# Optimization experiments

Hardware: AMD Instinct MI355X
Metric: run time of the kernel (lower is better)

## Reference

```python
import jax, jax.numpy as jnp
import numpy as np

B, T, C = 256, 168, 1024
N_SEQ = 168
HORIZON = 24


def setup_inputs() -> dict:
    key = jax.random.key(0)
    k1, k2, k3, k4 = jax.random.split(key, 4)
    x = jax.random.normal(k1, (B, T, C), dtype=jnp.float32)
    y = jax.random.normal(k2, (B, T, C), dtype=jnp.float32)
    # nn.Linear(n_seq, 1): weight [1, n_seq], bias [1]
    w = jax.random.normal(k3, (1, N_SEQ), dtype=jnp.float32) / jnp.sqrt(jnp.float32(N_SEQ))
    b = jax.random.normal(k4, (1,), dtype=jnp.float32) * 0.01
    return {"x": x, "y": y, "w": w, "b": b}


def reference(x, y, w, b):
    # x is unused in the original torch forward.
    n_seq = w.shape[1]
    yt = jnp.transpose(y, (0, 2, 1))          # [B, C, T]
    buf0 = yt[:, :, -n_seq:]                  # rolling window [B, C, n_seq]
    wv = w[0]                                 # [n_seq]
    bv = b[0]

    def step(buf, _):
        pred = jnp.einsum('bcn,n->bc', buf, wv) + bv   # [B, C]
        buf = jnp.concatenate([buf[:, :, 1:], pred[:, :, None]], axis=2)
        return buf, pred

    _, preds = jax.lax.scan(step, buf0, None, length=HORIZON)  # [H, B, C]
    # equivalent to y[:, :, -horizon:].permute(0, 2, 1) -> [B, H, C]
    return jnp.transpose(preds, (1, 0, 2))
```

## Files before the change

### kernel.cpp

```cpp
#include <hip/hip_runtime.h>

#define B_ 256
#define T_ 168
#define C_ 1024
#define H_ 24


__global__ __launch_bounds__(192) void ar_precompute(const float* __restrict__ w,
                                                     const float* __restrict__ bias,
                                                     float* __restrict__ ws) {
    __shared__ float lw[T_];
    const int t = threadIdx.x;
    if (t < T_) lw[t] = w[t];
    __syncthreads();
    if (t < T_) {
        float col[H_];
        #pragma unroll
        for (int k = 0; k < H_; ++k) {
            float v = (t >= k) ? lw[t - k] : 0.0f;
            #pragma unroll
            for (int j = 0; j < k; ++j)
                v += lw[T_ - k + j] * col[j];
            col[k] = v;
        }
        #pragma unroll
        for (int k = 0; k < H_; ++k)
            ws[t * H_ + k] = col[k];
    } else if (t == T_) {
        float bv = bias[0];
        float beta[H_];
        #pragma unroll
        for (int k = 0; k < H_; ++k) {
            float v = bv;
            #pragma unroll
            for (int j = 0; j < k; ++j)
                v += lw[T_ - k + j] * beta[j];
            beta[k] = v;
        }
        #pragma unroll
        for (int k = 0; k < H_; ++k)
            ws[T_ * H_ + k] = beta[k];
    }
}

__global__ __launch_bounds__(256) void ar_main(const float* __restrict__ y,
                                               const float* __restrict__ ws,
                                               float* __restrict__ out) {
    const int c = blockIdx.x * 256 + threadIdx.x;
    const int b = blockIdx.y;
    const float* __restrict__ yp = y + (size_t)b * (size_t)(T_ * C_) + c;
    const float* __restrict__ beta = ws + T_ * H_;

    float acc[H_];
    #pragma unroll
    for (int k = 0; k < H_; ++k) acc[k] = beta[k];

    #pragma unroll 4
    for (int t = 0; t < T_; ++t) {
        const float yv = yp[(size_t)t * C_];
        const float4* __restrict__ w4 = (const float4*)(ws + t * H_);
        #pragma unroll
        for (int q = 0; q < H_ / 4; ++q) {
            const float4 wv = w4[q];
            acc[4 * q + 0] += wv.x * yv;
            acc[4 * q + 1] += wv.y * yv;
            acc[4 * q + 2] += wv.z * yv;
            acc[4 * q + 3] += wv.w * yv;
        }
    }

    float* __restrict__ op = out + ((size_t)b * H_) * C_ + c;
    #pragma unroll
    for (int k = 0; k < H_; ++k)
        op[(size_t)k * C_] = acc[k];
}

extern "C" void kernel_launch(void* const* d_in, const int* in_sizes, int n_in,
                              void* d_out, int out_size, void* d_ws, size_t ws_size,
                              hipStream_t stream) {
    const float* y    = (const float*)d_in[1];
    const float* w    = (const float*)d_in[2];
    const float* bias = (const float*)d_in[3];
    float* out = (float*)d_out;
    float* ws  = (float*)d_ws;

    ar_precompute<<<1, 192, 0, stream>>>(w, bias, ws);
    ar_main<<<dim3(C_ / 256, B_), 256, 0, stream>>>(y, ws, out);
}
```

Measured before the change: 44.22 us.

## Fuse weight-propagation precompute into main kernel with shared-memory coefficients

Merges the single-block precompute kernel into the main kernel, so every block recomputes the unrolled horizon coefficient matrix and bias terms into shared memory before accumulating. This removes one kernel launch, the serial dependency between launches and the global workspace round trip. In exchange, each of the 1024 blocks redundantly does the O(T·H²) precompute, which adds per-block latency before the streaming loop, and the coefficient reads now come from LDS instead of cached global memory.

```diff
diff --git a/kernel.cpp b/kernel.cpp
--- a/kernel.cpp
+++ b/kernel.cpp
@@ -5,19 +5,23 @@
 #define C_ 1024
 #define H_ 24
 
+__global__ __launch_bounds__(256) void ar_fused(const float* __restrict__ y,
+                                                const float* __restrict__ w,
+                                                const float* __restrict__ bias,
+                                                float* __restrict__ out) {
+    __shared__ float lw[T_];
+    __shared__ float sW[T_ * H_];
+    __shared__ float sbeta[H_];
 
-__global__ __launch_bounds__(192) void ar_precompute(const float* __restrict__ w,
-                                                     const float* __restrict__ bias,
-                                                     float* __restrict__ ws) {
-    __shared__ float lw[T_];
-    const int t = threadIdx.x;
-    if (t < T_) lw[t] = w[t];
+    const int tid = threadIdx.x;
+    if (tid < T_) lw[tid] = w[tid];
     __syncthreads();
-    if (t < T_) {
+
+    if (tid < T_) {
         float col[H_];
         #pragma unroll
         for (int k = 0; k < H_; ++k) {
-            float v = (t >= k) ? lw[t - k] : 0.0f;
+            float v = (tid >= k) ? lw[tid - k] : 0.0f;
             #pragma unroll
             for (int j = 0; j < k; ++j)
                 v += lw[T_ - k + j] * col[j];
@@ -25,8 +29,8 @@
         }
         #pragma unroll
         for (int k = 0; k < H_; ++k)
-            ws[t * H_ + k] = col[k];
-    } else if (t == T_) {
+            sW[tid * H_ + k] = col[k];
+    } else if (tid == T_) {
         float bv = bias[0];
         float beta[H_];
         #pragma unroll
@@ -39,26 +43,22 @@
         }
         #pragma unroll
         for (int k = 0; k < H_; ++k)
-            ws[T_ * H_ + k] = beta[k];
+            sbeta[k] = beta[k];
     }
-}
+    __syncthreads();
 
-__global__ __launch_bounds__(256) void ar_main(const float* __restrict__ y,
-                                               const float* __restrict__ ws,
-                                               float* __restrict__ out) {
-    const int c = blockIdx.x * 256 + threadIdx.x;
+    const int c = blockIdx.x * 256 + tid;
     const int b = blockIdx.y;
     const float* __restrict__ yp = y + (size_t)b * (size_t)(T_ * C_) + c;
-    const float* __restrict__ beta = ws + T_ * H_;
 
     float acc[H_];
     #pragma unroll
-    for (int k = 0; k < H_; ++k) acc[k] = beta[k];
+    for (int k = 0; k < H_; ++k) acc[k] = sbeta[k];
 
     #pragma unroll 4
     for (int t = 0; t < T_; ++t) {
         const float yv = yp[(size_t)t * C_];
-        const float4* __restrict__ w4 = (const float4*)(ws + t * H_);
+        const float4* __restrict__ w4 = (const float4*)(sW + t * H_);
         #pragma unroll
         for (int q = 0; q < H_ / 4; ++q) {
             const float4 wv = w4[q];
@@ -82,8 +82,6 @@
     const float* w    = (const float*)d_in[2];
     const float* bias = (const float*)d_in[3];
     float* out = (float*)d_out;
-    float* ws  = (float*)d_ws;
 
-    ar_precompute<<<1, 192, 0, stream>>>(w, bias, ws);
-    ar_main<<<dim3(C_ / 256, B_), 256, 0, stream>>>(y, ws, out);
+    ar_fused<<<dim3(C_ / 256, B_), 256, 0, stream>>>(y, w, bias, out);
 }
```

After: 47.82 us. 8.1% more time.

## Split time reduction across two half-blocks and combine partial sums via LDS

Applied to the files above, without the earlier changes.

Each 256-thread block now covers 128 channels, and its two halves each reduce 84 of the 168 time steps. The second half writes its 24 partial accumulators to shared memory and the first half adds them plus the bias before storing. The grid doubles to 2048 blocks, giving more wavefronts and memory parallelism for the bandwidth-bound read of y. The cost is an LDS round trip, a barrier, and half the threads sitting idle during the final store.

```diff
diff --git a/kernel.cpp b/kernel.cpp
--- a/kernel.cpp
+++ b/kernel.cpp
@@ -4,6 +4,7 @@
 #define T_ 168
 #define C_ 1024
 #define H_ 24
+#define TH 84
 
 
 __global__ __launch_bounds__(192) void ar_precompute(const float* __restrict__ w,
@@ -43,22 +44,28 @@
     }
 }
 
-__global__ __launch_bounds__(256) void ar_main(const float* __restrict__ y,
-                                               const float* __restrict__ ws,
-                                               float* __restrict__ out) {
-    const int c = blockIdx.x * 256 + threadIdx.x;
+__global__ __launch_bounds__(256, 8) void ar_main(const float* __restrict__ y,
+                                                  const float* __restrict__ ws,
+                                                  float* __restrict__ out) {
+    __shared__ float sacc[H_ * 128];
+
+    const int tid = threadIdx.x;
+    const int c_local = tid & 127;
+    const int h = __builtin_amdgcn_readfirstlane(tid >> 7);
+
+    const int c = blockIdx.x * 128 + c_local;
     const int b = blockIdx.y;
-    const float* __restrict__ yp = y + (size_t)b * (size_t)(T_ * C_) + c;
-    const float* __restrict__ beta = ws + T_ * H_;
+    const float* __restrict__ yp =
+        y + (size_t)b * (size_t)(T_ * C_) + (size_t)(h * TH) * C_ + c;
 
     float acc[H_];
     #pragma unroll
-    for (int k = 0; k < H_; ++k) acc[k] = beta[k];
+    for (int k = 0; k < H_; ++k) acc[k] = 0.0f;
 
     #pragma unroll 4
-    for (int t = 0; t < T_; ++t) {
-        const float yv = yp[(size_t)t * C_];
-        const float4* __restrict__ w4 = (const float4*)(ws + t * H_);
+    for (int tt = 0; tt < TH; ++tt) {
+        const float yv = yp[(size_t)tt * C_];
+        const float4* __restrict__ w4 = (const float4*)(ws + (h * TH + tt) * H_);
         #pragma unroll
         for (int q = 0; q < H_ / 4; ++q) {
             const float4 wv = w4[q];
@@ -69,10 +76,19 @@
         }
     }
 
-    float* __restrict__ op = out + ((size_t)b * H_) * C_ + c;
-    #pragma unroll
-    for (int k = 0; k < H_; ++k)
-        op[(size_t)k * C_] = acc[k];
+    if (h == 1) {
+        #pragma unroll
+        for (int k = 0; k < H_; ++k)
+            sacc[k * 128 + c_local] = acc[k];
+    }
+    __syncthreads();
+    if (h == 0) {
+        const float* __restrict__ beta = ws + T_ * H_;
+        float* __restrict__ op = out + ((size_t)b * H_) * C_ + c;
+        #pragma unroll
+        for (int k = 0; k < H_; ++k)
+            op[(size_t)k * C_] = acc[k] + sacc[k * 128 + c_local] + beta[k];
+    }
 }
 
 extern "C" void kernel_launch(void* const* d_in, const int* in_sizes, int n_in,
@@ -85,5 +101,5 @@
     float* ws  = (float*)d_ws;
 
     ar_precompute<<<1, 192, 0, stream>>>(w, bias, ws);
-    ar_main<<<dim3(C_ / 256, B_), 256, 0, stream>>>(y, ws, out);
+    ar_main<<<dim3(C_ / 128, B_), 256, 0, stream>>>(y, ws, out);
 }
```

Measured after the change: 40.85 us. -7.6%, faster.
